# Optimization experiments

Measured on AMD Instinct MI355X. Metric: run time of the kernel, lower is better.

## Reference

```python
import jax, jax.numpy as jnp
import numpy as np

N, B, LMAX, DIM, IMG_DIM, LY, H = 32768, 16, 2560, 512, 768, 256, 8


def _layernorm(x, g, b, eps=1e-5):
    mu = jnp.mean(x, axis=-1, keepdims=True)
    var = jnp.mean(jnp.square(x - mu), axis=-1, keepdims=True)
    return (x - mu) * jax.lax.rsqrt(var + eps) * g + b


def setup_inputs() -> dict:
    key = jax.random.key(0)
    ks = jax.random.split(key, 16)
    s = DIM ** -0.5
    # ragged per-batch counts summing to N, all <= LMAX
    counts = np.full(B, N // B, dtype=np.int64)
    counts[: B // 2] += 200
    counts[B // 2:] -= 200
    batch_ids = jnp.asarray(np.repeat(np.arange(B), counts), dtype=jnp.int32)
    return {
        "F": jax.random.normal(ks[0], (N, DIM), jnp.float32),
        "y": jax.random.normal(ks[1], (B, LY, IMG_DIM), jnp.float32),
        "ln_g": jnp.ones((DIM,), jnp.float32),
        "ln_b": jnp.zeros((DIM,), jnp.float32),
        "Wq": jax.random.normal(ks[2], (DIM, DIM), jnp.float32) * s,
        "Wk": jax.random.normal(ks[3], (DIM, DIM), jnp.float32) * s,
        "Wv": jax.random.normal(ks[4], (DIM, DIM), jnp.float32) * s,
        "bq": jnp.zeros((DIM,), jnp.float32),
        "bk": jnp.zeros((DIM,), jnp.float32),
        "bv": jnp.zeros((DIM,), jnp.float32),
        "Wo": jax.random.normal(ks[5], (DIM, DIM), jnp.float32) * s,
        "bo": jnp.zeros((DIM,), jnp.float32),
        "W1": jax.random.normal(ks[6], (DIM, IMG_DIM), jnp.float32) * (IMG_DIM ** -0.5),
        "b1": jnp.zeros((DIM,), jnp.float32),
        "W2": jax.random.normal(ks[7], (DIM, DIM), jnp.float32) * s,
        "b2": jnp.zeros((DIM,), jnp.float32),
        "batch_ids": batch_ids,
        "Lmax": LMAX,
    }


def reference(F, y, ln_g, ln_b, Wq, Wk, Wv, bq, bk, bv, Wo, bo, W1, b1, W2, b2, batch_ids, Lmax):
    Bb, Ly, _ = y.shape
    n, dim = F.shape
    dh = dim // H
    # sparse -> dense: per-token slot index within its batch (batch_ids sorted)
    offsets = jnp.searchsorted(batch_ids, jnp.arange(Bb, dtype=batch_ids.dtype))
    pos = jnp.arange(n, dtype=jnp.int32) - offsets[batch_ids].astype(jnp.int32)
    xd = jnp.zeros((Bb, Lmax, dim), F.dtype).at[batch_ids, pos].set(F)  # [B,Lmax,D]
    # NOTE: self.norm is re-bound in subclass => same LayerNorm used twice
    xd = _layernorm(xd, ln_g, ln_b)
    # MLP fuse of image features: Linear -> GELU(exact) -> Linear
    ym = jax.nn.gelu(y @ W1.T + b1, approximate=False) @ W2.T + b2  # [B,Ly,D]
    # MHA cross-attention (no key_padding_mask: mask arg defaults to None)
    q = (xd @ Wq.T + bq).reshape(Bb, Lmax, H, dh)
    k = (ym @ Wk.T + bk).reshape(Bb, Ly, H, dh)
    v = (ym @ Wv.T + bv).reshape(Bb, Ly, H, dh)
    scores = jnp.einsum("bqhd,bkhd->bhqk", q, k) * (dh ** -0.5)
    attn = jax.nn.softmax(scores, axis=-1)
    o = jnp.einsum("bhqk,bkhd->bqhd", attn, v).reshape(Bb, Lmax, dim)
    o = o @ Wo.T + bo
    out_dense = _layernorm(xd + o, ln_g, ln_b)
    # dense -> sparse gather (equivalent to x_dense[x_mask])
    return out_dense[batch_ids, pos]
```

## Files before the change

### kernel.cpp

```cpp
#include <hip/hip_runtime.h>
#include <stdint.h>

#define NTOK 32768
#define BD   512
#define NB   16
#define LYK  256
#define IMGD 768

typedef __attribute__((ext_vector_type(4))) float f32x4;
typedef __attribute__((ext_vector_type(8))) short s16x8;
typedef unsigned short u16;

__device__ __forceinline__ float bf2f(u16 u) {
  union { uint32_t i; float f; } v; v.i = ((uint32_t)u) << 16; return v.f;
}
__device__ __forceinline__ u16 f2bf(float f) {
  union { float f; uint32_t i; } v; v.f = f;
  uint32_t r = v.i + 0x7fffu + ((v.i >> 16) & 1u);
  return (u16)(r >> 16);
}
__device__ __forceinline__ void gl_lds16(const u16* g, u16* l) {
  __builtin_amdgcn_global_load_lds(
      (const __attribute__((address_space(1))) uint32_t*)g,
      (__attribute__((address_space(3))) uint32_t*)l, 16, 0, 0);
}
__device__ __forceinline__ f32x4 mfma16(s16x8 a, s16x8 b, f32x4 c) {
  return __builtin_amdgcn_mfma_f32_16x16x32_bf16(a, b, c, 0, 0, 0);
}

__global__ __launch_bounds__(256) void cvt_f32_bf16(const float* __restrict__ s,
                                                    u16* __restrict__ d, int n) {
  int i = (blockIdx.x * 256 + threadIdx.x) * 8;
  if (i >= n) return;
  f32x4 a = *(const f32x4*)(s + i);
  f32x4 b = *(const f32x4*)(s + i + 4);
  s16x8 o;
#pragma unroll
  for (int j = 0; j < 4; ++j) { o[j] = (short)f2bf(a[j]); o[4 + j] = (short)f2bf(b[j]); }
  *(s16x8*)(d + i) = o;
}

__global__ void calc_off(const int* __restrict__ bids, int* __restrict__ off) {
  int b = threadIdx.x;
  if (b > NB) return;
  int lo = 0, hi = NTOK;
  while (lo < hi) { int mid = (lo + hi) >> 1; if (bids[mid] < b) lo = mid + 1; else hi = mid; }
  off[b] = lo;
}

__global__ __launch_bounds__(256) void ln_f32_bf16(const float* __restrict__ X,
                                                   const float* __restrict__ g,
                                                   const float* __restrict__ be,
                                                   u16* __restrict__ out) {
  const int lane = threadIdx.x & 63;
  const size_t row = (size_t)blockIdx.x * 4 + (threadIdx.x >> 6);
  const float* x = X + row * BD + lane * 8;
  f32x4 a = *(const f32x4*)x;
  f32x4 b = *(const f32x4*)(x + 4);
  float v[8] = {a[0], a[1], a[2], a[3], b[0], b[1], b[2], b[3]};
  float s = 0.f, s2 = 0.f;
#pragma unroll
  for (int j = 0; j < 8; ++j) { s += v[j]; s2 += v[j] * v[j]; }
#pragma unroll
  for (int m = 1; m < 64; m <<= 1) { s += __shfl_xor(s, m); s2 += __shfl_xor(s2, m); }
  float mean = s * (1.f / BD);
  float rstd = rsqrtf(s2 * (1.f / BD) - mean * mean + 1e-5f);
  const float* gp = g + lane * 8;
  const float* bp = be + lane * 8;
  s16x8 o;
#pragma unroll
  for (int j = 0; j < 8; ++j) o[j] = (short)f2bf((v[j] - mean) * rstd * gp[j] + bp[j]);
  *(s16x8*)(out + row * BD + lane * 8) = o;
}

__global__ __launch_bounds__(256) void ln_bf16_f32(const u16* __restrict__ Z,
                                                   const float* __restrict__ g,
                                                   const float* __restrict__ be,
                                                   float* __restrict__ out) {
  const int lane = threadIdx.x & 63;
  const size_t row = (size_t)blockIdx.x * 4 + (threadIdx.x >> 6);
  s16x8 zv = *(const s16x8*)(Z + row * BD + lane * 8);
  float v[8];
#pragma unroll
  for (int j = 0; j < 8; ++j) v[j] = bf2f((u16)zv[j]);
  float s = 0.f, s2 = 0.f;
#pragma unroll
  for (int j = 0; j < 8; ++j) { s += v[j]; s2 += v[j] * v[j]; }
#pragma unroll
  for (int m = 1; m < 64; m <<= 1) { s += __shfl_xor(s, m); s2 += __shfl_xor(s2, m); }
  float mean = s * (1.f / BD);
  float rstd = rsqrtf(s2 * (1.f / BD) - mean * mean + 1e-5f);
  const float* gp = g + lane * 8;
  const float* bp = be + lane * 8;
  f32x4 o0, o1;
#pragma unroll
  for (int j = 0; j < 4; ++j) o0[j] = (v[j] - mean) * rstd * gp[j] + bp[j];
#pragma unroll
  for (int j = 0; j < 4; ++j) o1[j] = (v[4 + j] - mean) * rstd * gp[4 + j] + bp[4 + j];
  float* op = out + row * BD + lane * 8;
  *(f32x4*)op = o0;
  *(f32x4*)(op + 4) = o1;
}

template <int EPI>
__global__ __launch_bounds__(256, 2) void gemm_nt(const u16* __restrict__ A,
                                                  const u16* __restrict__ W,
                                                  const float* __restrict__ bias,
                                                  u16* __restrict__ C,
                                                  const u16* __restrict__ resid, int K) {
  __shared__ u16 As[128 * 32];
  __shared__ u16 Bs[128 * 32];
  const int tid = threadIdx.x;
  const int wave = tid >> 6, lane = tid & 63;
  const int wm = (wave & 1) * 64, wn = (wave >> 1) * 64;
  const int quad = lane >> 4, l16 = lane & 15;
  const int m0 = blockIdx.x * 128, n0 = blockIdx.y * 128;

  f32x4 acc[4][4];
#pragma unroll
  for (int i = 0; i < 4; ++i)
#pragma unroll
    for (int j = 0; j < 4; ++j) acc[i][j] = f32x4{0.f, 0.f, 0.f, 0.f};

  const int srow = wave * 32 + (lane >> 2);
  const int scol = (lane & 3) * 8;
  const u16* gA0 = A + (size_t)(m0 + srow) * K + scol;
  const u16* gA1 = gA0 + (size_t)16 * K;
  const u16* gW0 = W + (size_t)(n0 + srow) * K + scol;
  const u16* gW1 = gW0 + (size_t)16 * K;
  u16* lA = As + wave * 1024;
  u16* lB = Bs + wave * 1024;

  for (int k0 = 0; k0 < K; k0 += 32) {
    __syncthreads();
    gl_lds16(gA0 + k0, lA);
    gl_lds16(gA1 + k0, lA + 512);
    gl_lds16(gW0 + k0, lB);
    gl_lds16(gW1 + k0, lB + 512);
    __syncthreads();
    s16x8 af[4], bfr[4];
#pragma unroll
    for (int mt = 0; mt < 4; ++mt)
      af[mt] = *(const s16x8*)&As[(wm + mt * 16 + l16) * 32 + quad * 8];
#pragma unroll
    for (int nt = 0; nt < 4; ++nt)
      bfr[nt] = *(const s16x8*)&Bs[(wn + nt * 16 + l16) * 32 + quad * 8];
#pragma unroll
    for (int mt = 0; mt < 4; ++mt)
#pragma unroll
      for (int nt = 0; nt < 4; ++nt)
        acc[mt][nt] = mfma16(af[mt], bfr[nt], acc[mt][nt]);
  }

#pragma unroll
  for (int nt = 0; nt < 4; ++nt) {
    const int n = n0 + wn + nt * 16 + l16;
    const float bia = bias[n];
#pragma unroll
    for (int mt = 0; mt < 4; ++mt) {
      const int mb = m0 + wm + mt * 16 + quad * 4;
#pragma unroll
      for (int r = 0; r < 4; ++r) {
        float v = acc[mt][nt][r] + bia;
        size_t idx = (size_t)(mb + r) * BD + n;
        if (EPI == 1) v = 0.5f * v * (1.f + erff(v * 0.70710678118654752f));
        if (EPI == 2) v += bf2f(resid[idx]);
        C[idx] = f2bf(v);
      }
    }
  }
}

__global__ __launch_bounds__(256, 2) void attn_k(const u16* __restrict__ Q,
                                                 const u16* __restrict__ Kg,
                                                 const u16* __restrict__ Vg,
                                                 const int* __restrict__ off,
                                                 u16* __restrict__ O) {
  const int t = blockIdx.x, h = blockIdx.y, b = blockIdx.z;
  const int qend = off[b + 1];
  const int qstart = off[b] + t * 64;
  if (qstart >= qend) return;

  __shared__ u16 KP[256 * 88];
  __shared__ u16 Vt[64 * 264];

  const int tid = threadIdx.x;
  const int wave = tid >> 6, lane = tid & 63;
  const int quad = lane >> 4, l16 = lane & 15;

  {
    const u16* src = Kg + ((size_t)b * LYK) * BD + h * 64;
#pragma unroll
    for (int s = 0; s < 8; ++s) {
      int seg = tid + s * 256;
      int l = seg >> 3, c8 = (seg & 7) * 8;
      *(s16x8*)&KP[l * 88 + c8] = *(const s16x8*)&src[(size_t)l * BD + c8];
    }
  }
  {
    const u16* src = Vg + ((size_t)b * LYK) * BD + h * 64;
    int d = tid & 63, lg = tid >> 6;
    for (int l = lg * 64; l < lg * 64 + 64; ++l)
      Vt[d * 264 + l] = src[(size_t)l * BD + d];
  }
  int qrow = qstart + wave * 16 + l16;
  if (qrow > NTOK - 1) qrow = NTOK - 1;
  const u16* qp = Q + (size_t)qrow * BD + h * 64 + quad * 8;
  s16x8 aq0 = *(const s16x8*)qp;
  s16x8 aq1 = *(const s16x8*)(qp + 32);

  __syncthreads();

  f32x4 sacc[16];
#pragma unroll
  for (int nt = 0; nt < 16; ++nt) sacc[nt] = f32x4{0.f, 0.f, 0.f, 0.f};
#pragma unroll
  for (int nt = 0; nt < 16; ++nt) {
    const u16* kp = &KP[(nt * 16 + l16) * 88 + quad * 8];
    s16x8 b0 = *(const s16x8*)kp;
    s16x8 b1 = *(const s16x8*)(kp + 32);
    sacc[nt] = mfma16(aq0, b0, sacc[nt]);
    sacc[nt] = mfma16(aq1, b1, sacc[nt]);
  }

  float inv[4];
#pragma unroll
  for (int r = 0; r < 4; ++r) {
    float m = -1e30f;
#pragma unroll
    for (int nt = 0; nt < 16; ++nt) m = fmaxf(m, sacc[nt][r]);
#pragma unroll
    for (int msk = 1; msk < 16; msk <<= 1) m = fmaxf(m, __shfl_xor(m, msk));
    float sum = 0.f;
#pragma unroll
    for (int nt = 0; nt < 16; ++nt) {
      float p = __expf(0.125f * (sacc[nt][r] - m));
      sacc[nt][r] = p;
      sum += p;
    }
#pragma unroll
    for (int msk = 1; msk < 16; msk <<= 1) sum += __shfl_xor(sum, msk);
    inv[r] = 1.f / sum;
  }

  __syncthreads();

  u16* Pw = KP + wave * (16 * 264);
#pragma unroll
  for (int nt = 0; nt < 16; ++nt)
#pragma unroll
    for (int r = 0; r < 4; ++r)
      Pw[(quad * 4 + r) * 264 + nt * 16 + l16] = f2bf(sacc[nt][r] * inv[r]);

  f32x4 oacc[4];
#pragma unroll
  for (int n2 = 0; n2 < 4; ++n2) oacc[n2] = f32x4{0.f, 0.f, 0.f, 0.f};
#pragma unroll
  for (int kc = 0; kc < 8; ++kc) {
    s16x8 ap = *(const s16x8*)&Pw[l16 * 264 + kc * 32 + quad * 8];
#pragma unroll
    for (int n2 = 0; n2 < 4; ++n2) {
      s16x8 bv = *(const s16x8*)&Vt[(n2 * 16 + l16) * 264 + kc * 32 + quad * 8];
      oacc[n2] = mfma16(ap, bv, oacc[n2]);
    }
  }

#pragma unroll
  for (int n2 = 0; n2 < 4; ++n2)
#pragma unroll
    for (int r = 0; r < 4; ++r) {
      int q = qstart + wave * 16 + quad * 4 + r;
      if (q < qend)
        O[(size_t)q * BD + h * 64 + n2 * 16 + l16] = f2bf(oacc[n2][r]);
    }
}

extern "C" void kernel_launch(void* const* d_in, const int* in_sizes, int n_in,
                              void* d_out, int out_size, void* d_ws, size_t ws_size,
                              hipStream_t stream) {
  const float* F    = (const float*)d_in[0];
  const float* yIn  = (const float*)d_in[1];
  const float* ln_g = (const float*)d_in[2];
  const float* ln_b = (const float*)d_in[3];
  const float* Wq   = (const float*)d_in[4];
  const float* Wk   = (const float*)d_in[5];
  const float* Wv   = (const float*)d_in[6];
  const float* bq   = (const float*)d_in[7];
  const float* bk   = (const float*)d_in[8];
  const float* bv   = (const float*)d_in[9];
  const float* Wo   = (const float*)d_in[10];
  const float* bo   = (const float*)d_in[11];
  const float* W1   = (const float*)d_in[12];
  const float* b1   = (const float*)d_in[13];
  const float* W2   = (const float*)d_in[14];
  const float* b2   = (const float*)d_in[15];
  const int* bids   = (const int*)d_in[16];

  char* ws = (char*)d_ws;
  size_t cur = 0;
  auto alloc = [&](size_t bytes) {
    void* p = ws + cur;
    cur += (bytes + 255) & ~(size_t)255;
    return p;
  };

  int* off  = (int*)alloc(68);
  u16* wq_b = (u16*)alloc((size_t)262144 * 2);
  u16* wk_b = (u16*)alloc((size_t)262144 * 2);
  u16* wv_b = (u16*)alloc((size_t)262144 * 2);
  u16* wo_b = (u16*)alloc((size_t)262144 * 2);
  u16* w2_b = (u16*)alloc((size_t)262144 * 2);
  u16* w1_b = (u16*)alloc((size_t)393216 * 2);
  u16* y_b  = (u16*)alloc((size_t)3145728 * 2);
  u16* U    = (u16*)alloc((size_t)4096 * BD * 2);
  u16* ym   = (u16*)alloc((size_t)4096 * BD * 2);
  u16* Kb   = (u16*)alloc((size_t)4096 * BD * 2);
  u16* Vb   = (u16*)alloc((size_t)4096 * BD * 2);
  u16* xn   = (u16*)alloc((size_t)NTOK * BD * 2);
  u16* Qb   = (u16*)alloc((size_t)NTOK * BD * 2);
  u16* Ob   = (u16*)alloc((size_t)NTOK * BD * 2);
  u16* Zb   = (u16*)alloc((size_t)NTOK * BD * 2);

  calc_off<<<1, 64, 0, stream>>>(bids, off);
  cvt_f32_bf16<<<262144 / 2048, 256, 0, stream>>>(Wq, wq_b, 262144);
  cvt_f32_bf16<<<262144 / 2048, 256, 0, stream>>>(Wk, wk_b, 262144);
  cvt_f32_bf16<<<262144 / 2048, 256, 0, stream>>>(Wv, wv_b, 262144);
  cvt_f32_bf16<<<262144 / 2048, 256, 0, stream>>>(Wo, wo_b, 262144);
  cvt_f32_bf16<<<262144 / 2048, 256, 0, stream>>>(W2, w2_b, 262144);
  cvt_f32_bf16<<<393216 / 2048, 256, 0, stream>>>(W1, w1_b, 393216);
  cvt_f32_bf16<<<3145728 / 2048, 256, 0, stream>>>(yIn, y_b, 3145728);
  ln_f32_bf16<<<NTOK / 4, 256, 0, stream>>>(F, ln_g, ln_b, xn);

  gemm_nt<1><<<dim3(32, 4), 256, 0, stream>>>(y_b, w1_b, b1, U, nullptr, IMGD);
  gemm_nt<0><<<dim3(32, 4), 256, 0, stream>>>(U, w2_b, b2, ym, nullptr, BD);
  gemm_nt<0><<<dim3(32, 4), 256, 0, stream>>>(ym, wk_b, bk, Kb, nullptr, BD);
  gemm_nt<0><<<dim3(32, 4), 256, 0, stream>>>(ym, wv_b, bv, Vb, nullptr, BD);
  gemm_nt<0><<<dim3(256, 4), 256, 0, stream>>>(xn, wq_b, bq, Qb, nullptr, BD);
  attn_k<<<dim3(40, 8, NB), 256, 0, stream>>>(Qb, Kb, Vb, off, Ob);
  gemm_nt<2><<<dim3(256, 4), 256, 0, stream>>>(Ob, wo_b, bo, Zb, xn, BD);
  ln_bf16_f32<<<NTOK / 4, 256, 0, stream>>>(Zb, ln_g, ln_b, (float*)d_out);
}
```

Measured before the change: 401.1 us.

## Fuse conversions and K/V projections, write V transposed, slim attention LDS

All seven fp32-to-bf16 conversion launches are merged into one kernel. The K and V projections become a single GEMM over a concatenated weight, and its epilogue writes V already transposed per batch, so attention reads V fragments straight from global memory instead of building a transposed copy in LDS with scalar stores. Attention drops the Vt shared buffer, shrinks the K padding, applies softmax normalisation after P·V, raises the occupancy hint and launches fewer tiles (36 instead of 40 along the query axis). The small image-side GEMMs switch to 64-row tiles for more blocks. In exchange, the transposed-V writes are strided and V reads in attention now come from global memory or cache instead of LDS.

```diff
diff --git a/kernel.cpp b/kernel.cpp
--- a/kernel.cpp
+++ b/kernel.cpp
@@ -9,6 +9,7 @@
 
 typedef __attribute__((ext_vector_type(4))) float f32x4;
 typedef __attribute__((ext_vector_type(8))) short s16x8;
+typedef __attribute__((ext_vector_type(4))) unsigned short u16x4;
 typedef unsigned short u16;
 
 __device__ __forceinline__ float bf2f(u16 u) {
@@ -28,10 +29,23 @@
   return __builtin_amdgcn_mfma_f32_16x16x32_bf16(a, b, c, 0, 0, 0);
 }
 
-__global__ __launch_bounds__(256) void cvt_f32_bf16(const float* __restrict__ s,
-                                                    u16* __restrict__ d, int n) {
-  int i = (blockIdx.x * 256 + threadIdx.x) * 8;
-  if (i >= n) return;
+__global__ __launch_bounds__(256) void cvt_all(
+    const float* __restrict__ wq, const float* __restrict__ wk,
+    const float* __restrict__ wv, const float* __restrict__ wo,
+    const float* __restrict__ w2, const float* __restrict__ w1,
+    const float* __restrict__ y,
+    u16* __restrict__ dq, u16* __restrict__ dkv, u16* __restrict__ dwo,
+    u16* __restrict__ dw2, u16* __restrict__ dw1, u16* __restrict__ dy) {
+  int bid = blockIdx.x;
+  const float* s; u16* d; int base;
+  if      (bid < 128)  { s = wq; d = dq;            base = 0;   }
+  else if (bid < 256)  { s = wk; d = dkv;           base = 128; }
+  else if (bid < 384)  { s = wv; d = dkv + 262144;  base = 256; }
+  else if (bid < 512)  { s = wo; d = dwo;           base = 384; }
+  else if (bid < 640)  { s = w2; d = dw2;           base = 512; }
+  else if (bid < 832)  { s = w1; d = dw1;           base = 640; }
+  else                 { s = y;  d = dy;            base = 832; }
+  int i = ((bid - base) * 256 + threadIdx.x) * 8;
   f32x4 a = *(const f32x4*)(s + i);
   f32x4 b = *(const f32x4*)(s + i + 4);
   s16x8 o;
@@ -102,78 +116,93 @@
   *(f32x4*)(op + 4) = o1;
 }
 
-template <int EPI>
+template <int TM, int EPI>
 __global__ __launch_bounds__(256, 2) void gemm_nt(const u16* __restrict__ A,
                                                   const u16* __restrict__ W,
                                                   const float* __restrict__ bias,
                                                   u16* __restrict__ C,
-                                                  const u16* __restrict__ resid, int K) {
-  __shared__ u16 As[128 * 32];
+                                                  const u16* __restrict__ resid,
+                                                  u16* __restrict__ C2,
+                                                  const float* __restrict__ bias2,
+                                                  int K) {
+  constexpr int MT = 4;
+  constexpr int NT = (TM == 128) ? 4 : 2;
+  __shared__ u16 As[TM * 32];
   __shared__ u16 Bs[128 * 32];
   const int tid = threadIdx.x;
   const int wave = tid >> 6, lane = tid & 63;
-  const int wm = (wave & 1) * 64, wn = (wave >> 1) * 64;
+  const int wm = (TM == 128) ? (wave & 1) * 64 : 0;
+  const int wn = (TM == 128) ? (wave >> 1) * 64 : wave * 32;
   const int quad = lane >> 4, l16 = lane & 15;
-  const int m0 = blockIdx.x * 128, n0 = blockIdx.y * 128;
-
-  f32x4 acc[4][4];
-#pragma unroll
-  for (int i = 0; i < 4; ++i)
-#pragma unroll
-    for (int j = 0; j < 4; ++j) acc[i][j] = f32x4{0.f, 0.f, 0.f, 0.f};
-
-  const int srow = wave * 32 + (lane >> 2);
+  const int m0 = blockIdx.x * TM, n0 = blockIdx.y * 128;
+
+  f32x4 acc[MT][NT];
+#pragma unroll
+  for (int i = 0; i < MT; ++i)
+#pragma unroll
+    for (int j = 0; j < NT; ++j) acc[i][j] = f32x4{0.f, 0.f, 0.f, 0.f};
+
   const int scol = (lane & 3) * 8;
-  const u16* gA0 = A + (size_t)(m0 + srow) * K + scol;
+  const int srowA = (TM == 128) ? wave * 32 + (lane >> 2) : wave * 16 + (lane >> 2);
+  const int srowB = wave * 32 + (lane >> 2);
+  const u16* gA0 = A + (size_t)(m0 + srowA) * K + scol;
   const u16* gA1 = gA0 + (size_t)16 * K;
-  const u16* gW0 = W + (size_t)(n0 + srow) * K + scol;
+  const u16* gW0 = W + (size_t)(n0 + srowB) * K + scol;
   const u16* gW1 = gW0 + (size_t)16 * K;
-  u16* lA = As + wave * 1024;
+  u16* lA = As + ((TM == 128) ? wave * 1024 : wave * 512);
   u16* lB = Bs + wave * 1024;
 
   for (int k0 = 0; k0 < K; k0 += 32) {
     __syncthreads();
     gl_lds16(gA0 + k0, lA);
-    gl_lds16(gA1 + k0, lA + 512);
+    if (TM == 128) gl_lds16(gA1 + k0, lA + 512);
     gl_lds16(gW0 + k0, lB);
     gl_lds16(gW1 + k0, lB + 512);
     __syncthreads();
-    s16x8 af[4], bfr[4];
-#pragma unroll
-    for (int mt = 0; mt < 4; ++mt)
+    s16x8 af[MT], bfr[NT];
+#pragma unroll
+    for (int mt = 0; mt < MT; ++mt)
       af[mt] = *(const s16x8*)&As[(wm + mt * 16 + l16) * 32 + quad * 8];
 #pragma unroll
-    for (int nt = 0; nt < 4; ++nt)
+    for (int nt = 0; nt < NT; ++nt)
       bfr[nt] = *(const s16x8*)&Bs[(wn + nt * 16 + l16) * 32 + quad * 8];
 #pragma unroll
-    for (int mt = 0; mt < 4; ++mt)
-#pragma unroll
-      for (int nt = 0; nt < 4; ++nt)
+    for (int mt = 0; mt < MT; ++mt)
+#pragma unroll
+      for (int nt = 0; nt < NT; ++nt)
         acc[mt][nt] = mfma16(af[mt], bfr[nt], acc[mt][nt]);
   }
 
 #pragma unroll
-  for (int nt = 0; nt < 4; ++nt) {
+  for (int nt = 0; nt < NT; ++nt) {
     const int n = n0 + wn + nt * 16 + l16;
-    const float bia = bias[n];
-#pragma unroll
-    for (int mt = 0; mt < 4; ++mt) {
+    const float bia = (EPI == 3) ? (n < BD ? bias[n] : bias2[n - BD]) : bias[n];
+#pragma unroll
+    for (int mt = 0; mt < MT; ++mt) {
       const int mb = m0 + wm + mt * 16 + quad * 4;
-#pragma unroll
-      for (int r = 0; r < 4; ++r) {
-        float v = acc[mt][nt][r] + bia;
-        size_t idx = (size_t)(mb + r) * BD + n;
-        if (EPI == 1) v = 0.5f * v * (1.f + erff(v * 0.70710678118654752f));
-        if (EPI == 2) v += bf2f(resid[idx]);
-        C[idx] = f2bf(v);
+      if (EPI == 3 && n >= BD) {
+        u16x4 pk;
+#pragma unroll
+        for (int r = 0; r < 4; ++r) pk[r] = f2bf(acc[mt][nt][r] + bia);
+        const int b = mb >> 8, k0i = mb & 255;
+        *(u16x4*)&C2[((size_t)b * BD + (n - BD)) * LYK + k0i] = pk;
+      } else {
+#pragma unroll
+        for (int r = 0; r < 4; ++r) {
+          float v = acc[mt][nt][r] + bia;
+          size_t idx = (size_t)(mb + r) * BD + n;
+          if (EPI == 1) v = 0.5f * v * (1.f + erff(v * 0.70710678118654752f));
+          if (EPI == 2) v += bf2f(resid[idx]);
+          C[idx] = f2bf(v);
+        }
       }
     }
   }
 }
 
-__global__ __launch_bounds__(256, 2) void attn_k(const u16* __restrict__ Q,
+__global__ __launch_bounds__(256, 4) void attn_k(const u16* __restrict__ Q,
                                                  const u16* __restrict__ Kg,
-                                                 const u16* __restrict__ Vg,
+                                                 const u16* __restrict__ VT,
                                                  const int* __restrict__ off,
                                                  u16* __restrict__ O) {
   const int t = blockIdx.x, h = blockIdx.y, b = blockIdx.z;
@@ -181,8 +210,7 @@
   const int qstart = off[b] + t * 64;
   if (qstart >= qend) return;
 
-  __shared__ u16 KP[256 * 88];
-  __shared__ u16 Vt[64 * 264];
+  __shared__ u16 KP[256 * 72];
 
   const int tid = threadIdx.x;
   const int wave = tid >> 6, lane = tid & 63;
@@ -194,14 +222,8 @@
     for (int s = 0; s < 8; ++s) {
       int seg = tid + s * 256;
       int l = seg >> 3, c8 = (seg & 7) * 8;
-      *(s16x8*)&KP[l * 88 + c8] = *(const s16x8*)&src[(size_t)l * BD + c8];
-    }
-  }
-  {
-    const u16* src = Vg + ((size_t)b * LYK) * BD + h * 64;
-    int d = tid & 63, lg = tid >> 6;
-    for (int l = lg * 64; l < lg * 64 + 64; ++l)
-      Vt[d * 264 + l] = src[(size_t)l * BD + d];
+      *(s16x8*)&KP[l * 72 + c8] = *(const s16x8*)&src[(size_t)l * BD + c8];
+    }
   }
   int qrow = qstart + wave * 16 + l16;
   if (qrow > NTOK - 1) qrow = NTOK - 1;
@@ -216,7 +238,7 @@
   for (int nt = 0; nt < 16; ++nt) sacc[nt] = f32x4{0.f, 0.f, 0.f, 0.f};
 #pragma unroll
   for (int nt = 0; nt < 16; ++nt) {
-    const u16* kp = &KP[(nt * 16 + l16) * 88 + quad * 8];
+    const u16* kp = &KP[(nt * 16 + l16) * 72 + quad * 8];
     s16x8 b0 = *(const s16x8*)kp;
     s16x8 b1 = *(const s16x8*)(kp + 32);
     sacc[nt] = mfma16(aq0, b0, sacc[nt]);
@@ -250,8 +272,9 @@
   for (int nt = 0; nt < 16; ++nt)
 #pragma unroll
     for (int r = 0; r < 4; ++r)
-      Pw[(quad * 4 + r) * 264 + nt * 16 + l16] = f2bf(sacc[nt][r] * inv[r]);
-
+      Pw[(quad * 4 + r) * 264 + nt * 16 + l16] = f2bf(sacc[nt][r]);
+
+  const u16* vb = VT + ((size_t)b * BD + h * 64) * LYK;
   f32x4 oacc[4];
 #pragma unroll
   for (int n2 = 0; n2 < 4; ++n2) oacc[n2] = f32x4{0.f, 0.f, 0.f, 0.f};
@@ -260,7 +283,7 @@
     s16x8 ap = *(const s16x8*)&Pw[l16 * 264 + kc * 32 + quad * 8];
 #pragma unroll
     for (int n2 = 0; n2 < 4; ++n2) {
-      s16x8 bv = *(const s16x8*)&Vt[(n2 * 16 + l16) * 264 + kc * 32 + quad * 8];
+      s16x8 bv = *(const s16x8*)&vb[(size_t)(n2 * 16 + l16) * LYK + kc * 32 + quad * 8];
       oacc[n2] = mfma16(ap, bv, oacc[n2]);
     }
   }
@@ -271,7 +294,7 @@
     for (int r = 0; r < 4; ++r) {
       int q = qstart + wave * 16 + quad * 4 + r;
       if (q < qend)
-        O[(size_t)q * BD + h * 64 + n2 * 16 + l16] = f2bf(oacc[n2][r]);
+        O[(size_t)q * BD + h * 64 + n2 * 16 + l16] = f2bf(oacc[n2][r] * inv[r]);
     }
 }
 
@@ -304,39 +327,32 @@
     return p;
   };
 
-  int* off  = (int*)alloc(68);
-  u16* wq_b = (u16*)alloc((size_t)262144 * 2);
-  u16* wk_b = (u16*)alloc((size_t)262144 * 2);
-  u16* wv_b = (u16*)alloc((size_t)262144 * 2);
-  u16* wo_b = (u16*)alloc((size_t)262144 * 2);
-  u16* w2_b = (u16*)alloc((size_t)262144 * 2);
-  u16* w1_b = (u16*)alloc((size_t)393216 * 2);
-  u16* y_b  = (u16*)alloc((size_t)3145728 * 2);
-  u16* U    = (u16*)alloc((size_t)4096 * BD * 2);
-  u16* ym   = (u16*)alloc((size_t)4096 * BD * 2);
-  u16* Kb   = (u16*)alloc((size_t)4096 * BD * 2);
-  u16* Vb   = (u16*)alloc((size_t)4096 * BD * 2);
-  u16* xn   = (u16*)alloc((size_t)NTOK * BD * 2);
-  u16* Qb   = (u16*)alloc((size_t)NTOK * BD * 2);
-  u16* Ob   = (u16*)alloc((size_t)NTOK * BD * 2);
-  u16* Zb   = (u16*)alloc((size_t)NTOK * BD * 2);
+  int* off   = (int*)alloc(68);
+  u16* wq_b  = (u16*)alloc((size_t)262144 * 2);
+  u16* wkv_b = (u16*)alloc((size_t)524288 * 2);
+  u16* wo_b  = (u16*)alloc((size_t)262144 * 2);
+  u16* w2_b  = (u16*)alloc((size_t)262144 * 2);
+  u16* w1_b  = (u16*)alloc((size_t)393216 * 2);
+  u16* y_b   = (u16*)alloc((size_t)3145728 * 2);
+  u16* U     = (u16*)alloc((size_t)4096 * BD * 2);
+  u16* ym    = (u16*)alloc((size_t)4096 * BD * 2);
+  u16* Kb    = (u16*)alloc((size_t)4096 * BD * 2);
+  u16* VT    = (u16*)alloc((size_t)NB * BD * LYK * 2);
+  u16* xn    = (u16*)alloc((size_t)NTOK * BD * 2);
+  u16* Qb    = (u16*)alloc((size_t)NTOK * BD * 2);
+  u16* Ob    = (u16*)alloc((size_t)NTOK * BD * 2);
+  u16* Zb    = (u16*)alloc((size_t)NTOK * BD * 2);
 
   calc_off<<<1, 64, 0, stream>>>(bids, off);
-  cvt_f32_bf16<<<262144 / 2048, 256, 0, stream>>>(Wq, wq_b, 262144);
-  cvt_f32_bf16<<<262144 / 2048, 256, 0, stream>>>(Wk, wk_b, 262144);
-  cvt_f32_bf16<<<262144 / 2048, 256, 0, stream>>>(Wv, wv_b, 262144);
-  cvt_f32_bf16<<<262144 / 2048, 256, 0, stream>>>(Wo, wo_b, 262144);
-  cvt_f32_bf16<<<262144 / 2048, 256, 0, stream>>>(W2, w2_b, 262144);
-  cvt_f32_bf16<<<393216 / 2048, 256, 0, stream>>>(W1, w1_b, 393216);
-  cvt_f32_bf16<<<3145728 / 2048, 256, 0, stream>>>(yIn, y_b, 3145728);
+  cvt_all<<<2368, 256, 0, stream>>>(Wq, Wk, Wv, Wo, W2, W1, yIn,
+                                    wq_b, wkv_b, wo_b, w2_b, w1_b, y_b);
   ln_f32_bf16<<<NTOK / 4, 256, 0, stream>>>(F, ln_g, ln_b, xn);
 
-  gemm_nt<1><<<dim3(32, 4), 256, 0, stream>>>(y_b, w1_b, b1, U, nullptr, IMGD);
-  gemm_nt<0><<<dim3(32, 4), 256, 0, stream>>>(U, w2_b, b2, ym, nullptr, BD);
-  gemm_nt<0><<<dim3(32, 4), 256, 0, stream>>>(ym, wk_b, bk, Kb, nullptr, BD);
-  gemm_nt<0><<<dim3(32, 4), 256, 0, stream>>>(ym, wv_b, bv, Vb, nullptr, BD);
-  gemm_nt<0><<<dim3(256, 4), 256, 0, stream>>>(xn, wq_b, bq, Qb, nullptr, BD);
-  attn_k<<<dim3(40, 8, NB), 256, 0, stream>>>(Qb, Kb, Vb, off, Ob);
-  gemm_nt<2><<<dim3(256, 4), 256, 0, stream>>>(Ob, wo_b, bo, Zb, xn, BD);
+  gemm_nt<64, 1><<<dim3(64, 4), 256, 0, stream>>>(y_b, w1_b, b1, U, nullptr, nullptr, nullptr, IMGD);
+  gemm_nt<64, 0><<<dim3(64, 4), 256, 0, stream>>>(U, w2_b, b2, ym, nullptr, nullptr, nullptr, BD);
+  gemm_nt<128, 3><<<dim3(32, 8), 256, 0, stream>>>(ym, wkv_b, bk, Kb, nullptr, VT, bv, BD);
+  gemm_nt<128, 0><<<dim3(256, 4), 256, 0, stream>>>(xn, wq_b, bq, Qb, nullptr, nullptr, nullptr, BD);
+  attn_k<<<dim3(36, 8, NB), 256, 0, stream>>>(Qb, Kb, VT, off, Ob);
+  gemm_nt<128, 2><<<dim3(256, 4), 256, 0, stream>>>(Ob, wo_b, bo, Zb, xn, nullptr, nullptr, BD);
   ln_bf16_f32<<<NTOK / 4, 256, 0, stream>>>(Zb, ln_g, ln_b, (float*)d_out);
 }
```

New measurement: 398.2 us. About the same (-0.7%).
